# Performance work log

Hardware: AMD Instinct MI355X
Metric: run time of the kernel (lower is better)

The kernel has to match this reference:

```python
import jax, jax.numpy as jnp
import numpy as np

D = 1024      # d_model
B = 8         # batch
S = 512       # seq
L = 2         # GRU layers
DEPTH = 3     # min_depth == max_depth -> fixed recursion depth
EPS_RMS = 1.1920929e-07  # torch fp32 finfo eps (nn.RMSNorm default)


def setup_inputs() -> dict:
    key = jax.random.key(0)
    ks = jax.random.split(key, 16)

    def glorot(k, shape):
        fan_out, fan_in = shape
        lim = float(np.sqrt(6.0 / (fan_in + fan_out)))
        return jax.random.uniform(k, shape, jnp.float32, -lim, lim)

    gs = float(1.0 / np.sqrt(D))  # torch GRU init: U(-1/sqrt(H), 1/sqrt(H))
    inp = {
        "x": jax.random.normal(ks[0], (B, S, D), jnp.float32),
        # reflect: Linear -> RMSNorm -> GELU -> Linear -> RMSNorm
        "w1": glorot(ks[1], (D, D)), "b1": jnp.zeros(D, jnp.float32),
        "rms1_w": jnp.ones(D, jnp.float32),
        "w2": glorot(ks[2], (D, D)), "b2": jnp.zeros(D, jnp.float32),
        "rms2_w": jnp.ones(D, jnp.float32),
        "residual_weight": jnp.float32(0.5),
        # IntegrationMeasure projections (xavier_uniform, zero bias)
        "whole_w": glorot(ks[3], (D // 2, D)), "whole_b": jnp.zeros(D // 2, jnp.float32),
        "parts_w": glorot(ks[4], (D // 2, D)), "parts_b": jnp.zeros(D // 2, jnp.float32),
        "phi_scale": jnp.float32(1.0), "phi_bias": jnp.float32(0.0),
    }
    ki = 5
    for l in range(L):
        inp[f"wih{l}"] = jax.random.uniform(ks[ki + 0], (3 * D, D), jnp.float32, -gs, gs)
        inp[f"whh{l}"] = jax.random.uniform(ks[ki + 1], (3 * D, D), jnp.float32, -gs, gs)
        inp[f"bih{l}"] = jax.random.uniform(ks[ki + 2], (3 * D,), jnp.float32, -gs, gs)
        inp[f"bhh{l}"] = jax.random.uniform(ks[ki + 3], (3 * D,), jnp.float32, -gs, gs)
        ki += 4
    return inp


def _rmsnorm(x, w):
    ms = jnp.mean(x * x, axis=-1, keepdims=True)
    return x * jax.lax.rsqrt(ms + EPS_RMS) * w


def _gru_layer(seq, h0, Wih, Whh, bih, bhh):
    """seq: [S,B,D], h0: [B,D] -> (outputs [S,B,D], h_final [B,D]). torch gate order r,z,n."""
    def step(h, xt):
        gi = xt @ Wih.T + bih                       # [B, 3D]
        gh = h @ Whh.T + bhh                        # [B, 3D]
        ir, iz, ig = jnp.split(gi, 3, axis=-1)
        hr, hz, hg = jnp.split(gh, 3, axis=-1)
        r = jax.nn.sigmoid(ir + hr)
        z = jax.nn.sigmoid(iz + hz)
        n = jnp.tanh(ig + r * hg)
        hn = (1.0 - z) * n + z * h
        return hn, hn
    hT, ys = jax.lax.scan(step, h0, seq)
    return ys, hT


def reference(x, w1, b1, rms1_w, w2, b2, rms2_w, residual_weight,
              wih0, whh0, bih0, bhh0, wih1, whh1, bih1, bhh1,
              whole_w, whole_b, parts_w, parts_b, phi_scale, phi_bias):
    gru = [(wih0, whh0, bih0, bhh0), (wih1, whh1, bih1, bhh1)]
    batch = x.shape[0]
    hidden = [jnp.zeros((batch, D), x.dtype) for _ in range(L)]
    history = []  # detached states
    phi = None

    for loop in range(DEPTH):
        # self-reflection block
        h = _rmsnorm(x @ w1.T + b1, rms1_w)
        h = jax.nn.gelu(h, approximate=False)
        h = _rmsnorm(h @ w2.T + b2, rms2_w)
        x_ref = x + residual_weight * (h - x)
        # GRU integration (seq-first)
        seq = jnp.transpose(x_ref, (1, 0, 2))       # [S,B,D]
        new_hidden = []
        for l in range(L):
            seq, hT = _gru_layer(seq, hidden[l], *gru[l])
            new_hidden.append(hT)
        hidden = new_hidden
        x = jnp.transpose(seq, (0, 1, 2)).transpose(1, 0, 2)  # [B,S,D]
        # Phi (IntegrationMeasure) -- manifold_norm == L2 norm, fully vectorized
        whole = x @ whole_w.T + whole_b             # [B,S,D/2]
        whole_info = jnp.linalg.norm(whole, axis=-1).mean(axis=-1)  # [B]
        if len(history) == 0:
            phi = jnp.broadcast_to(jax.nn.sigmoid(phi_bias) * 0.3, (batch,))
        else:
            parts = jnp.stack(history) @ parts_w.T + parts_b      # [H,B,S,D/2]
            parts_info = jnp.linalg.norm(parts, axis=-1).mean(axis=-1).mean(axis=0)  # [B]
            raw_phi = (whole_info - parts_info) / (whole_info + 1e-08)
            phi = jnp.clip(phi_scale * raw_phi + phi_bias, 0.0, 1.0)
        history.append(jax.lax.stop_gradient(x))    # torch: x.clone().detach()

    return x, phi
```

## Files before the change

### kernel.cpp

```cpp
#include <hip/hip_runtime.h>
#include <math.h>

#define Dm 1024
#define Bm 8
#define Sm 512

typedef short s16x8 __attribute__((ext_vector_type(8)));
typedef float f32x4 __attribute__((ext_vector_type(4)));
typedef unsigned short u16;
typedef unsigned long long u64;

__device__ __forceinline__ float bf2f(u16 u) {
  union { float f; unsigned v; } x; x.v = (unsigned)u << 16; return x.f;
}
__device__ __forceinline__ u16 f2bf(float f) {
  union { float f; unsigned v; } x; x.f = f;
  unsigned r = x.v + 0x7FFFu + ((x.v >> 16) & 1u);
  return (u16)(r >> 16);
}
__device__ __forceinline__ float sigm(float x) { return 1.f / (1.f + expf(-x)); }

__device__ __forceinline__ u64 cld64(const void* p) {
  return __hip_atomic_load((const u64*)p, __ATOMIC_RELAXED, __HIP_MEMORY_SCOPE_AGENT);
}
__device__ __forceinline__ float cldf(const void* p) {
  return __hip_atomic_load((const float*)p, __ATOMIC_RELAXED, __HIP_MEMORY_SCOPE_AGENT);
}
__device__ __forceinline__ void cx64(void* p, u64 v) {
  u64 old = __hip_atomic_exchange((u64*)p, v, __ATOMIC_RELAXED, __HIP_MEMORY_SCOPE_AGENT);
  asm volatile("" :: "v"(old));
}
__device__ __forceinline__ void cst32(void* p, unsigned v) {
  __hip_atomic_store((unsigned*)p, v, __ATOMIC_RELAXED, __HIP_MEMORY_SCOPE_AGENT);
}

__global__ void k_conv(const float* __restrict__ x, const float* __restrict__ w1,
                       const float* __restrict__ w2, const float* __restrict__ ww,
                       const float* __restrict__ pw,
                       u16* __restrict__ Xb, u16* __restrict__ Wc,
                       float* __restrict__ Hf, u16* __restrict__ Hb,
                       float* __restrict__ sums, unsigned* __restrict__ flags,
                       unsigned* __restrict__ poison)
{
  long gid = (long)blockIdx.x * blockDim.x + threadIdx.x;
  const long N0 = 4194304, N1 = 1048576, N2 = 1048576, N3 = 524288, N4 = 524288;
  const long T = N0 + N1 + N2 + N3 + N4;
  for (long p = gid; p < T; p += (long)gridDim.x * blockDim.x) {
    long q = p;
    if (q < N0) { Xb[q] = f2bf(x[q]); continue; }
    q -= N0;
    if (q < N1) { Wc[q] = f2bf(w1[q]); continue; }
    q -= N1;
    if (q < N2) { Wc[N1 + q] = f2bf(w2[q]); continue; }
    q -= N2;
    if (q < N3) { Wc[N1 + N2 + q] = f2bf(ww[q]); continue; }
    q -= N3;
    Wc[N1 + N2 + N3 + q] = f2bf(pw[q]);
  }
  if (gid < 65536) flags[gid] = 0;
  if (gid < 2 * Bm * Dm) Hf[gid] = 0.f;
  if (gid < 262144) Hb[gid] = 0;
  if (gid < 16) sums[gid] = 0.f;
  if (gid == 0) *poison = 0;
}

template<int MODE>
__global__ __launch_bounds__(512)
void k_gemm(const u16* __restrict__ A, const u16* __restrict__ W,
            const float* __restrict__ bias, const float* __restrict__ nw,
            const u16* __restrict__ XresB, const float* __restrict__ rwp,
            u16* __restrict__ out0, float* __restrict__ sumdst, int Ncols)
{
  __shared__ u16 At[16 * 1024];
  __shared__ float rowsq[16];
  const int tid = threadIdx.x;
  const int lane = tid & 63, wv = tid >> 6;
  const int rlo = lane & 15, khi = lane >> 4;
  const int m0 = blockIdx.x * 16;

  {
    int row = tid & 15, c = tid >> 4;
    const char* src = (const char*)(A + (long)(m0 + row) * Dm);
    char* dst = (char*)At + row * 2048;
    int sw = (row & 7) << 4;
#pragma unroll
    for (int i = 0; i < 4; ++i) {
      int bo = c * 64 + i * 16;
      s16x8 v = *(const s16x8*)(src + bo);
      *(s16x8*)(dst + (bo ^ sw)) = v;
    }
  }
  __syncthreads();

  const int j0 = wv * 128;
  const bool act = j0 < Ncols;
  f32x4 zero4 = {0.f, 0.f, 0.f, 0.f};
  f32x4 acc[8];
#pragma unroll
  for (int jt = 0; jt < 8; ++jt) acc[jt] = zero4;

  if (act) {
    const u16* wbase = W + (long)(j0 + rlo) * Dm + khi * 8;
    const char* abase = (const char*)At + rlo * 2048;
    const int asw = (rlo & 7) << 4;
#pragma unroll
    for (int ks = 0; ks < 32; ++ks) {
      s16x8 a = *(const s16x8*)(abase + (((ks * 32 + khi * 8) * 2) ^ asw));
#pragma unroll
      for (int jt = 0; jt < 8; ++jt) {
        s16x8 b = *(const s16x8*)(wbase + (long)jt * 16 * Dm + ks * 32);
        acc[jt] = __builtin_amdgcn_mfma_f32_16x16x32_bf16(a, b, acc[jt], 0, 0, 0);
      }
    }
  }

  if (tid < 16) rowsq[tid] = 0.f;
  __syncthreads();

  float vals[8][4];
  if (act) {
    float rs[4] = {0.f, 0.f, 0.f, 0.f};
#pragma unroll
    for (int jt = 0; jt < 8; ++jt) {
      float bj = bias[j0 + jt * 16 + rlo];
#pragma unroll
      for (int r = 0; r < 4; ++r) {
        float v = acc[jt][r] + bj;
        vals[jt][r] = v;
        rs[r] += v * v;
      }
    }
#pragma unroll
    for (int r = 0; r < 4; ++r) {
#pragma unroll
      for (int m = 1; m < 16; m <<= 1) rs[r] += __shfl_xor(rs[r], m, 64);
    }
    if (rlo == 0) {
#pragma unroll
      for (int r = 0; r < 4; ++r) atomicAdd(&rowsq[khi * 4 + r], rs[r]);
    }
  }
  __syncthreads();

  if constexpr (MODE == 2) {
    if (tid < 16) {
      int token = m0 + tid;
      atomicAdd(&sumdst[token >> 9], sqrtf(rowsq[tid]));
    }
    return;
  } else {
    float rw = 0.f;
    if constexpr (MODE == 1) rw = rwp[0];
    if (act) {
#pragma unroll
      for (int jt = 0; jt < 8; ++jt) {
        int col = j0 + jt * 16 + rlo;
        float nwv = nw[col];
#pragma unroll
        for (int r = 0; r < 4; ++r) {
          int row = khi * 4 + r;
          int token = m0 + row;
          float ms = rowsq[row] * (1.f / 1024.f) + 1.1920929e-07f;
          float y = vals[jt][r] * rsqrtf(ms) * nwv;
          if constexpr (MODE == 0) {
            y = 0.5f * y * (1.f + erff(y * 0.7071067811865476f));
            out0[(long)token * Dm + col] = f2bf(y);
          } else {
            float xf = bf2f(XresB[(long)token * Dm + col]);
            float xr = xf + rw * (y - xf);
            u16 hi = f2bf(xr);
            float lo = xr - bf2f(hi);
            int s = token & (Sm - 1), b = token >> 9;
            long base = ((long)s * 16 + b) * Dm + col;
            out0[base] = hi;
            out0[base + 8 * Dm] = f2bf(lo);
          }
        }
      }
    }
  }
}

#define SPIN_CAP 2000000

__device__ __forceinline__ bool spin_all(const unsigned* pA, const unsigned* pB,
                                         unsigned val, unsigned* poison) {
  int spins = 0;
  while (true) {
    bool c = __hip_atomic_load(pA, __ATOMIC_RELAXED, __HIP_MEMORY_SCOPE_AGENT) >= val;
    if (pB) c = c && (__hip_atomic_load(pB, __ATOMIC_RELAXED, __HIP_MEMORY_SCOPE_AGENT) >= val);
    if (__all(c)) return true;
    __builtin_amdgcn_s_sleep(1);
    if ((++spins & 255) == 0) {
      if (__hip_atomic_load(poison, __ATOMIC_RELAXED, __HIP_MEMORY_SCOPE_AGENT)) return false;
      if (spins > SPIN_CAP) {
        __hip_atomic_store(poison, 1u, __ATOMIC_RELAXED, __HIP_MEMORY_SCOPE_AGENT);
        return false;
      }
    }
  }
}

__global__ __launch_bounds__(256, 1)
void k_rec(const float* __restrict__ wih0, const float* __restrict__ whh0,
           const float* __restrict__ bih0, const float* __restrict__ bhh0,
           const float* __restrict__ wih1, const float* __restrict__ whh1,
           const float* __restrict__ bih1, const float* __restrict__ bhh1,
           const u16* __restrict__ XrefB,
           float* __restrict__ gi0r, float* __restrict__ gi1r,
           u16* __restrict__ Hb, float* __restrict__ Hf,
           u16* __restrict__ Xb, float* __restrict__ outx,
           unsigned* __restrict__ flags, unsigned* __restrict__ poison, int loop)
{
  __shared__ u16 hbuf[16 * 1024];
  __shared__ float part[4][3][16][33];

  const int wg = blockIdx.x;
  const int role = wg >> 5;
  const int w = wg & 31;
  const int d0 = w * 32;
  const int tid = threadIdx.x;
  const int lane = tid & 63, q = tid >> 6;
  const int rlo = lane & 15, khi = lane >> 4;
  const unsigned val = (unsigned)loop + 1u;

  unsigned* F0 = flags;
  unsigned* F1 = flags + 16384;
  unsigned* F2 = flags + 32768;
  unsigned* F3 = flags + 49152;
  u16* Hb0 = Hb;
  u16* Hb1 = Hb + 8 * 16384;

  const float* Wsel = (role == 0) ? wih0 : (role == 1) ? whh0 : (role == 2) ? wih1 : whh1;

  s16x8 bfr[8][3][2];
#pragma unroll
  for (int ks = 0; ks < 8; ++ks)
#pragma unroll
    for (int g = 0; g < 3; ++g)
#pragma unroll
      for (int jt = 0; jt < 2; ++jt) {
        int rowj = g * 1024 + d0 + jt * 16 + rlo;
        const float* p = Wsel + (long)rowj * Dm + q * 256 + ks * 32 + khi * 8;
        s16x8 f;
#pragma unroll
        for (int e = 0; e < 8; ++e) f[e] = (short)f2bf(p[e]);
        bfr[ks][g][jt] = f;
      }

  const int ob = tid >> 5, odd = tid & 31, od = d0 + odd;
  float bias_r[3];
  {
    const float* bsel = (role == 0) ? bih0 : (role == 1) ? bhh0 : (role == 2) ? bih1 : bhh1;
#pragma unroll
    for (int g = 0; g < 3; ++g) bias_r[g] = bsel[g * 1024 + od];
  }
  const int layer = (role == 1) ? 0 : 1;
  float hreg = 0.f;
  if (role == 1 || role == 3) hreg = Hf[layer * 8192 + ob * 1024 + od];
  __syncthreads();

  for (int t = 0; t < Sm; ++t) {
    if (role == 0) {
      if (t >= 8) { if (!spin_all(&F1[(t - 8) * 32 + w], nullptr, val, poison)) return; }
    } else if (role == 1) {
      const unsigned* fb = &F0[t * 32 + w];
      const unsigned* pA =
          (lane < 32) ? ((t >= 1) ? &F1[(t - 1) * 32 + lane] : fb)
                      : ((t >= 8) ? &F2[(t - 8) * 32 + (lane - 32)] : fb);
      if (!spin_all(pA, fb, val, poison)) return;
    } else if (role == 2) {
      const unsigned* pA =
          (lane < 32) ? &F1[t * 32 + lane]
                      : ((t >= 8) ? &F3[(t - 8) * 32 + (lane - 32)] : &F1[t * 32 + (lane - 32)]);
      if (!spin_all(pA, nullptr, val, poison)) return;
    } else {
      const unsigned* fb = &F2[t * 32 + w];
      const unsigned* pA = (lane < 32) ? ((t >= 1) ? &F3[(t - 1) * 32 + lane] : fb) : fb;
      if (!spin_all(pA, fb, val, poison)) return;
    }
    __builtin_amdgcn_sched_barrier(0);

    float giv[3] = {0.f, 0.f, 0.f};
    if (role == 1 || role == 3) {
      const float* ring = ((role == 1) ? gi0r : gi1r) + ((long)(t & 7) * Bm + ob) * 3072 + od;
      giv[0] = cldf(ring);
      giv[1] = cldf(ring + 1024);
      giv[2] = cldf(ring + 2048);
    }
    __syncthreads();

    if (role == 0) {
      const u16* asrc = XrefB + (long)t * 16 * Dm;
      int row = tid & 15, c = tid >> 4;
      const char* src = (const char*)(asrc + row * Dm);
      char* dst = (char*)hbuf + row * 2048;
      int sw = (row & 7) << 4;
#pragma unroll
      for (int i = 0; i < 8; ++i) {
        int bo = c * 128 + i * 16;
        s16x8 v = *(const s16x8*)(src + bo);
        *(s16x8*)(dst + (bo ^ sw)) = v;
      }
    } else {
      const u16* asrc =
          (role == 1) ? Hb0 + ((t - 1) & 7) * 16384 :
          (role == 2) ? Hb0 + (t & 7) * 16384 :
                        Hb1 + ((t - 1) & 7) * 16384;
      int row = tid & 15, c = tid >> 4;
      const u16* src = asrc + row * 1024 + c * 64;
      char* dst = (char*)hbuf + row * 2048;
      int sw = (row & 7) << 4;
#pragma unroll
      for (int i = 0; i < 16; ++i) {
        u64 v = cld64(src + i * 4);
        int bo = c * 128 + i * 8;
        *(u64*)(dst + (bo ^ sw)) = v;
      }
    }
    __syncthreads();

    f32x4 zero4 = {0.f, 0.f, 0.f, 0.f};
    f32x4 acc[3][2];
#pragma unroll
    for (int g = 0; g < 3; ++g) { acc[g][0] = zero4; acc[g][1] = zero4; }
    const char* abase = (const char*)hbuf + rlo * 2048;
    const int asw = (rlo & 7) << 4;
#pragma unroll
    for (int ks = 0; ks < 8; ++ks) {
      s16x8 a = *(const s16x8*)(abase + (((q * 256 + ks * 32 + khi * 8) * 2) ^ asw));
#pragma unroll
      for (int g = 0; g < 3; ++g)
#pragma unroll
        for (int jt = 0; jt < 2; ++jt)
          acc[g][jt] = __builtin_amdgcn_mfma_f32_16x16x32_bf16(a, bfr[ks][g][jt], acc[g][jt], 0, 0, 0);
    }
#pragma unroll
    for (int g = 0; g < 3; ++g)
#pragma unroll
      for (int jt = 0; jt < 2; ++jt)
#pragma unroll
        for (int r = 0; r < 4; ++r)
          part[q][g][khi * 4 + r][jt * 16 + rlo] = acc[g][jt][r];
    __syncthreads();

    {
      int b = ob, dd = odd, d = od;
      float v[3];
#pragma unroll
      for (int g = 0; g < 3; ++g) {
        float sv = 0.f;
#pragma unroll
        for (int qq = 0; qq < 4; ++qq)
          sv += part[qq][g][b][dd] + part[qq][g][8 + b][dd];
        v[g] = sv;
      }
      if (role == 0 || role == 2) {
        float* ring = ((role == 0) ? gi0r : gi1r) + ((long)(t & 7) * Bm + b) * 3072 + d;
#pragma unroll
        for (int g = 0; g < 3; ++g) {
          float fg = v[g] + bias_r[g];
          float pg = __shfl_xor(fg, 1, 64);
          if ((dd & 1) == 0) {
            union { float f; unsigned u; } a0, a1;
            a0.f = fg; a1.f = pg;
            u64 pk = (u64)a0.u | ((u64)a1.u << 32);
            cx64(ring + g * 1024, pk);
          }
        }
      } else {
        float gr = giv[0] + v[0] + bias_r[0];
        float gz = giv[1] + v[1] + bias_r[1];
        float ghn = v[2] + bias_r[2];
        float rr = sigm(gr), zz = sigm(gz);
        float nn = tanhf(giv[2] + rr * ghn);
        float hn = (1.f - zz) * nn + zz * hreg;
        hreg = hn;
        u16 hi = f2bf(hn);
        u16 lo = f2bf(hn - bf2f(hi));
        unsigned myv = (unsigned)hi | ((unsigned)lo << 16);
        unsigned p1 = __shfl_xor(myv, 1, 64);
        unsigned hiPair = (myv & 0xFFFFu) | ((p1 & 0xFFFFu) << 16);
        unsigned loPair = (myv >> 16) | (p1 & 0xFFFF0000u);
        unsigned hp2 = __shfl_xor(hiPair, 2, 64);
        unsigned lp2 = __shfl_xor(loPair, 2, 64);
        if ((dd & 3) == 0) {
          u64 hq = (u64)hiPair | ((u64)hp2 << 32);
          u64 lq = (u64)loPair | ((u64)lp2 << 32);
          u16* hb = ((role == 1) ? Hb0 : Hb1) + (t & 7) * 16384;
          cx64(hb + b * 1024 + d, hq);
          cx64(hb + 8192 + b * 1024 + d, lq);
        }
        if (role == 3) {
          long xi = ((long)b * Sm + t) * Dm + d;
          Xb[xi] = hi;
          if (outx) outx[xi] = hn;
        }
        if (t == Sm - 1) Hf[layer * 8192 + b * 1024 + d] = hreg;
      }
    }
    __syncthreads();
    __builtin_amdgcn_sched_barrier(0);
    if (tid == 0) {
      unsigned* F = (role == 0) ? F0 : (role == 1) ? F1 : (role == 2) ? F2 : F3;
      cst32(&F[t * 32 + w], val);
    }
  }
}

__global__ void k_phi(const float* __restrict__ sums, const float* __restrict__ psc,
                      const float* __restrict__ pbi, float* __restrict__ out)
{
  int b = threadIdx.x;
  if (b < 8) {
    float whole = sums[8 + b] * (1.f / 512.f);
    float parts = sums[b] * (1.f / 1024.f);
    float raw = (whole - parts) / (whole + 1e-8f);
    float phi = psc[0] * raw + pbi[0];
    phi = fminf(fmaxf(phi, 0.f), 1.f);
    out[(long)Bm * Sm * Dm + b] = phi;
  }
}

extern "C" void kernel_launch(void* const* d_in, const int* in_sizes, int n_in,
                              void* d_out, int out_size, void* d_ws, size_t ws_size,
                              hipStream_t stream)
{
  (void)in_sizes; (void)n_in; (void)out_size;
  const float* b1   = (const float*)d_in[2];
  const float* r1w  = (const float*)d_in[3];
  const float* b2   = (const float*)d_in[5];
  const float* r2w  = (const float*)d_in[6];
  const float* rw   = (const float*)d_in[7];
  const float* wb   = (const float*)d_in[9];
  const float* pb   = (const float*)d_in[11];
  const float* psc  = (const float*)d_in[12];
  const float* pbi  = (const float*)d_in[13];
  const float* wih0 = (const float*)d_in[14];
  const float* whh0 = (const float*)d_in[15];
  const float* bih0 = (const float*)d_in[16];
  const float* bhh0 = (const float*)d_in[17];
  const float* wih1 = (const float*)d_in[18];
  const float* whh1 = (const float*)d_in[19];
  const float* bih1 = (const float*)d_in[20];
  const float* bhh1 = (const float*)d_in[21];
  float* out = (float*)d_out;

  if (ws_size < 45000000) return;

  char* ws = (char*)d_ws;
  size_t off = 0;
  auto alloc = [&](size_t bytes) -> char* {
    char* p = ws + off;
    off += (bytes + 255) & ~(size_t)255;
    return p;
  };
  u16*      Xb    = (u16*)  alloc((size_t)4194304 * 2);
  u16*      T1    = (u16*)  alloc((size_t)4194304 * 2);
  u16*      XrefB = (u16*)  alloc((size_t)2 * 4194304 * 2);
  float*    gi0r  = (float*)alloc((size_t)8 * 8 * 3072 * 4);
  float*    gi1r  = (float*)alloc((size_t)8 * 8 * 3072 * 4);
  u16*      Hb    = (u16*)  alloc((size_t)2 * 8 * 16384 * 2);
  float*    Hf    = (float*)alloc((size_t)2 * 8192 * 4);
  u16*      Wc    = (u16*)  alloc((size_t)3145728 * 2);
  float*    sums  = (float*)alloc(16 * 4);
  unsigned* flags = (unsigned*)alloc((size_t)65536 * 4);
  unsigned* poi   = (unsigned*)alloc(256);

  u16* WcW1 = Wc;
  u16* WcW2 = Wc + 1048576;
  u16* WcWW = Wc + 2097152;
  u16* WcPW = Wc + 2621440;

  k_conv<<<2048, 256, 0, stream>>>((const float*)d_in[0], (const float*)d_in[1],
                                   (const float*)d_in[4], (const float*)d_in[8],
                                   (const float*)d_in[10],
                                   Xb, Wc, Hf, Hb, sums, flags, poi);

  for (int loop = 0; loop < 3; ++loop) {
    k_gemm<0><<<256, 512, 0, stream>>>(Xb, WcW1, b1, r1w, nullptr, nullptr, T1, nullptr, 1024);
    k_gemm<1><<<256, 512, 0, stream>>>(T1, WcW2, b2, r2w, Xb, rw, XrefB, nullptr, 1024);
    k_rec<<<128, 256, 0, stream>>>(wih0, whh0, bih0, bhh0, wih1, whh1, bih1, bhh1,
                                   XrefB, gi0r, gi1r, Hb, Hf, Xb,
                                   (loop == 2) ? out : nullptr, flags, poi, loop);
    if (loop < 2)
      k_gemm<2><<<256, 512, 0, stream>>>(Xb, WcPW, pb, nullptr, nullptr, nullptr, nullptr, sums, 512);
    else
      k_gemm<2><<<256, 512, 0, stream>>>(Xb, WcWW, wb, nullptr, nullptr, nullptr, nullptr, sums + 8, 512);
  }
  k_phi<<<1, 64, 0, stream>>>(sums, psc, pbi, out);
}
```

Measured before the change: 12.40 ms.

## Merge input and hidden GRU projections into one workgroup per layer slice

The persistent recurrent kernel drops from four roles (input-proj and hidden-proj per layer) to two, with each workgroup holding both Wih and Whh fragments in registers and computing both projections for its slice. This removes the gi ring buffers in global memory and one level of cross-workgroup flag handoff per timestep, which shortens the serial dependency chain. In exchange it doubles register pressure for the weight fragments and the MFMA work per workgroup, and halves the number of active workgroups. Only one wave now spins on flags, and a shared-memory poison flag propagates an abort to the rest of the block.

```diff
diff --git a/kernel.cpp b/kernel.cpp
--- a/kernel.cpp
+++ b/kernel.cpp
@@ -22,9 +22,6 @@
 
 __device__ __forceinline__ u64 cld64(const void* p) {
   return __hip_atomic_load((const u64*)p, __ATOMIC_RELAXED, __HIP_MEMORY_SCOPE_AGENT);
-}
-__device__ __forceinline__ float cldf(const void* p) {
-  return __hip_atomic_load((const float*)p, __ATOMIC_RELAXED, __HIP_MEMORY_SCOPE_AGENT);
 }
 __device__ __forceinline__ void cx64(void* p, u64 v) {
   u64 old = __hip_atomic_exchange((u64*)p, v, __ATOMIC_RELAXED, __HIP_MEMORY_SCOPE_AGENT);
@@ -57,7 +54,7 @@
     q -= N3;
     Wc[N1 + N2 + N3 + q] = f2bf(pw[q]);
   }
-  if (gid < 65536) flags[gid] = 0;
+  if (gid < 32768) flags[gid] = 0;
   if (gid < 2 * Bm * Dm) Hf[gid] = 0.f;
   if (gid < 262144) Hb[gid] = 0;
   if (gid < 16) sums[gid] = 0.f;
@@ -183,12 +180,11 @@
 
 #define SPIN_CAP 2000000
 
-__device__ __forceinline__ bool spin_all(const unsigned* pA, const unsigned* pB,
-                                         unsigned val, unsigned* poison) {
+__device__ __forceinline__ bool spin_en(const unsigned* p, bool en, unsigned val,
+                                        unsigned* poison) {
   int spins = 0;
   while (true) {
-    bool c = __hip_atomic_load(pA, __ATOMIC_RELAXED, __HIP_MEMORY_SCOPE_AGENT) >= val;
-    if (pB) c = c && (__hip_atomic_load(pB, __ATOMIC_RELAXED, __HIP_MEMORY_SCOPE_AGENT) >= val);
+    bool c = !en || (__hip_atomic_load(p, __ATOMIC_RELAXED, __HIP_MEMORY_SCOPE_AGENT) >= val);
     if (__all(c)) return true;
     __builtin_amdgcn_s_sleep(1);
     if ((++spins & 255) == 0) {
@@ -207,13 +203,14 @@
            const float* __restrict__ wih1, const float* __restrict__ whh1,
            const float* __restrict__ bih1, const float* __restrict__ bhh1,
            const u16* __restrict__ XrefB,
-           float* __restrict__ gi0r, float* __restrict__ gi1r,
            u16* __restrict__ Hb, float* __restrict__ Hf,
            u16* __restrict__ Xb, float* __restrict__ outx,
            unsigned* __restrict__ flags, unsigned* __restrict__ poison, int loop)
 {
-  __shared__ u16 hbuf[16 * 1024];
-  __shared__ float part[4][3][16][33];
+  __shared__ u16 hbufI[16 * 1024];
+  __shared__ u16 hbufH[16 * 1024];
+  __shared__ float part[4][4][16][33];
+  __shared__ unsigned pflag;
 
   const int wg = blockIdx.x;
   const int role = wg >> 5;
@@ -224,16 +221,17 @@
   const int rlo = lane & 15, khi = lane >> 4;
   const unsigned val = (unsigned)loop + 1u;
 
-  unsigned* F0 = flags;
-  unsigned* F1 = flags + 16384;
-  unsigned* F2 = flags + 32768;
-  unsigned* F3 = flags + 49152;
+  unsigned* F1 = flags;
+  unsigned* F3 = flags + 16384;
   u16* Hb0 = Hb;
   u16* Hb1 = Hb + 8 * 16384;
 
-  const float* Wsel = (role == 0) ? wih0 : (role == 1) ? whh0 : (role == 2) ? wih1 : whh1;
-
-  s16x8 bfr[8][3][2];
+  if (tid == 0) pflag = 0;
+
+  const float* WI = role ? wih1 : wih0;
+  const float* WH = role ? whh1 : whh0;
+
+  s16x8 fI[8][3][2], fH[8][3][2];
 #pragma unroll
   for (int ks = 0; ks < 8; ++ks)
 #pragma unroll
@@ -241,60 +239,51 @@
 #pragma unroll
       for (int jt = 0; jt < 2; ++jt) {
         int rowj = g * 1024 + d0 + jt * 16 + rlo;
-        const float* p = Wsel + (long)rowj * Dm + q * 256 + ks * 32 + khi * 8;
-        s16x8 f;
-#pragma unroll
-        for (int e = 0; e < 8; ++e) f[e] = (short)f2bf(p[e]);
-        bfr[ks][g][jt] = f;
+        long boff = (long)rowj * Dm + q * 256 + ks * 32 + khi * 8;
+        const float* pI = WI + boff;
+        const float* pH = WH + boff;
+        s16x8 a, b;
+#pragma unroll
+        for (int e = 0; e < 8; ++e) { a[e] = (short)f2bf(pI[e]); b[e] = (short)f2bf(pH[e]); }
+        fI[ks][g][jt] = a;
+        fH[ks][g][jt] = b;
       }
 
   const int ob = tid >> 5, odd = tid & 31, od = d0 + odd;
-  float bias_r[3];
-  {
-    const float* bsel = (role == 0) ? bih0 : (role == 1) ? bhh0 : (role == 2) ? bih1 : bhh1;
-#pragma unroll
-    for (int g = 0; g < 3; ++g) bias_r[g] = bsel[g * 1024 + od];
-  }
-  const int layer = (role == 1) ? 0 : 1;
-  float hreg = 0.f;
-  if (role == 1 || role == 3) hreg = Hf[layer * 8192 + ob * 1024 + od];
+  const float* bI = role ? bih1 : bih0;
+  const float* bH = role ? bhh1 : bhh0;
+  float bias_r = bI[od] + bH[od];
+  float bias_z = bI[1024 + od] + bH[1024 + od];
+  float bias_ni = bI[2048 + od];
+  float bias_nh = bH[2048 + od];
+  float hreg = Hf[role * 8192 + ob * 1024 + od];
   __syncthreads();
 
   for (int t = 0; t < Sm; ++t) {
-    if (role == 0) {
-      if (t >= 8) { if (!spin_all(&F1[(t - 8) * 32 + w], nullptr, val, poison)) return; }
-    } else if (role == 1) {
-      const unsigned* fb = &F0[t * 32 + w];
-      const unsigned* pA =
-          (lane < 32) ? ((t >= 1) ? &F1[(t - 1) * 32 + lane] : fb)
-                      : ((t >= 8) ? &F2[(t - 8) * 32 + (lane - 32)] : fb);
-      if (!spin_all(pA, fb, val, poison)) return;
-    } else if (role == 2) {
-      const unsigned* pA =
-          (lane < 32) ? &F1[t * 32 + lane]
-                      : ((t >= 8) ? &F3[(t - 8) * 32 + (lane - 32)] : &F1[t * 32 + (lane - 32)]);
-      if (!spin_all(pA, nullptr, val, poison)) return;
-    } else {
-      const unsigned* fb = &F2[t * 32 + w];
-      const unsigned* pA = (lane < 32) ? ((t >= 1) ? &F3[(t - 1) * 32 + lane] : fb) : fb;
-      if (!spin_all(pA, fb, val, poison)) return;
+    if (q == 0) {
+      const unsigned* p;
+      bool en;
+      if (role == 0) {
+        int tm1 = (t >= 1) ? t - 1 : 0;
+        int tm8 = (t >= 8) ? t - 8 : 0;
+        p = (lane < 32) ? &F1[tm1 * 32 + lane] : &F3[tm8 * 32 + (lane - 32)];
+        en = (lane < 32) ? (t >= 1) : (t >= 8);
+      } else {
+        int sm1 = (t >= 1) ? t - 1 : 0;
+        p = (lane < 32) ? &F1[t * 32 + lane] : &F3[sm1 * 32 + (lane - 32)];
+        en = (lane < 32) ? true : (t >= 1);
+      }
+      if (!spin_en(p, en, val, poison)) { if (lane == 0) pflag = 1; }
     }
     __builtin_amdgcn_sched_barrier(0);
-
-    float giv[3] = {0.f, 0.f, 0.f};
-    if (role == 1 || role == 3) {
-      const float* ring = ((role == 1) ? gi0r : gi1r) + ((long)(t & 7) * Bm + ob) * 3072 + od;
-      giv[0] = cldf(ring);
-      giv[1] = cldf(ring + 1024);
-      giv[2] = cldf(ring + 2048);
-    }
     __syncthreads();
+    if (pflag) return;
 
     if (role == 0) {
       const u16* asrc = XrefB + (long)t * 16 * Dm;
       int row = tid & 15, c = tid >> 4;
       const char* src = (const char*)(asrc + row * Dm);
-      char* dst = (char*)hbuf + row * 2048;
+      char* dst = (char*)hbufI + row * 2048;
       int sw = (row & 7) << 4;
 #pragma unroll
       for (int i = 0; i < 8; ++i) {
@@ -303,13 +292,10 @@
         *(s16x8*)(dst + (bo ^ sw)) = v;
       }
     } else {
-      const u16* asrc =
-          (role == 1) ? Hb0 + ((t - 1) & 7) * 16384 :
-          (role == 2) ? Hb0 + (t & 7) * 16384 :
-                        Hb1 + ((t - 1) & 7) * 16384;
+      const u16* asrc = Hb0 + (t & 7) * 16384;
       int row = tid & 15, c = tid >> 4;
       const u16* src = asrc + row * 1024 + c * 64;
-      char* dst = (char*)hbuf + row * 2048;
+      char* dst = (char*)hbufI + row * 2048;
       int sw = (row & 7) << 4;
 #pragma unroll
       for (int i = 0; i < 16; ++i) {
@@ -318,91 +304,96 @@
         *(u64*)(dst + (bo ^ sw)) = v;
       }
     }
+    {
+      const u16* asrc = (role ? Hb1 : Hb0) + ((t - 1) & 7) * 16384;
+      int row = tid & 15, c = tid >> 4;
+      const u16* src = asrc + row * 1024 + c * 64;
+      char* dst = (char*)hbufH + row * 2048;
+      int sw = (row & 7) << 4;
+#pragma unroll
+      for (int i = 0; i < 16; ++i) {
+        u64 v = cld64(src + i * 4);
+        int bo = c * 128 + i * 8;
+        *(u64*)(dst + (bo ^ sw)) = v;
+      }
+    }
     __syncthreads();
 
     f32x4 zero4 = {0.f, 0.f, 0.f, 0.f};
-    f32x4 acc[3][2];
-#pragma unroll
-    for (int g = 0; g < 3; ++g) { acc[g][0] = zero4; acc[g][1] = zero4; }
-    const char* abase = (const char*)hbuf + rlo * 2048;
+    f32x4 accR[2], accZ[2], accNI[2], accNH[2];
+#pragma unroll
+    for (int jt = 0; jt < 2; ++jt) { accR[jt] = zero4; accZ[jt] = zero4; accNI[jt] = zero4; accNH[jt] = zero4; }
+    const char* aIb = (const char*)hbufI + rlo * 2048;
+    const char* aHb = (const char*)hbufH + rlo * 2048;
     const int asw = (rlo & 7) << 4;
 #pragma unroll
     for (int ks = 0; ks < 8; ++ks) {
-      s16x8 a = *(const s16x8*)(abase + (((q * 256 + ks * 32 + khi * 8) * 2) ^ asw));
-#pragma unroll
-      for (int g = 0; g < 3; ++g)
-#pragma unroll
-        for (int jt = 0; jt < 2; ++jt)
-          acc[g][jt] = __builtin_amdgcn_mfma_f32_16x16x32_bf16(a, bfr[ks][g][jt], acc[g][jt], 0, 0, 0);
-    }
-#pragma unroll
-    for (int g = 0; g < 3; ++g)
-#pragma unroll
-      for (int jt = 0; jt < 2; ++jt)
-#pragma unroll
-        for (int r = 0; r < 4; ++r)
-          part[q][g][khi * 4 + r][jt * 16 + rlo] = acc[g][jt][r];
+      int ao = (((q * 256 + ks * 32 + khi * 8) * 2)) ;
+      s16x8 aI = *(const s16x8*)(aIb + (ao ^ asw));
+      s16x8 aH = *(const s16x8*)(aHb + (ao ^ asw));
+#pragma unroll
+      for (int jt = 0; jt < 2; ++jt) {
+        accR[jt] = __builtin_amdgcn_mfma_f32_16x16x32_bf16(aI, fI[ks][0][jt], accR[jt], 0, 0, 0);
+        accR[jt] = __builtin_amdgcn_mfma_f32_16x16x32_bf16(aH, fH[ks][0][jt], accR[jt], 0, 0, 0);
+        accZ[jt] = __builtin_amdgcn_mfma_f32_16x16x32_bf16(aI, fI[ks][1][jt], accZ[jt], 0, 0, 0);
+        accZ[jt] = __builtin_amdgcn_mfma_f32_16x16x32_bf16(aH, fH[ks][1][jt], accZ[jt], 0, 0, 0);
+        accNI[jt] = __builtin_amdgcn_mfma_f32_16x16x32_bf16(aI, fI[ks][2][jt], accNI[jt], 0, 0, 0);
+        accNH[jt] = __builtin_amdgcn_mfma_f32_16x16x32_bf16(aH, fH[ks][2][jt], accNH[jt], 0, 0, 0);
+      }
+    }
+#pragma unroll
+    for (int jt = 0; jt < 2; ++jt)
+#pragma unroll
+      for (int r = 0; r < 4; ++r) {
+        part[q][0][khi * 4 + r][jt * 16 + rlo] = accR[jt][r];
+        part[q][1][khi * 4 + r][jt * 16 + rlo] = accZ[jt][r];
+        part[q][2][khi * 4 + r][jt * 16 + rlo] = accNI[jt][r];
+        part[q][3][khi * 4 + r][jt * 16 + rlo] = accNH[jt][r];
+      }
     __syncthreads();
 
     {
-      int b = ob, dd = odd, d = od;
-      float v[3];
-#pragma unroll
-      for (int g = 0; g < 3; ++g) {
+      int b = ob, dd = odd;
+      float v[4];
+#pragma unroll
+      for (int g = 0; g < 4; ++g) {
         float sv = 0.f;
 #pragma unroll
         for (int qq = 0; qq < 4; ++qq)
           sv += part[qq][g][b][dd] + part[qq][g][8 + b][dd];
         v[g] = sv;
       }
-      if (role == 0 || role == 2) {
-        float* ring = ((role == 0) ? gi0r : gi1r) + ((long)(t & 7) * Bm + b) * 3072 + d;
-#pragma unroll
-        for (int g = 0; g < 3; ++g) {
-          float fg = v[g] + bias_r[g];
-          float pg = __shfl_xor(fg, 1, 64);
-          if ((dd & 1) == 0) {
-            union { float f; unsigned u; } a0, a1;
-            a0.f = fg; a1.f = pg;
-            u64 pk = (u64)a0.u | ((u64)a1.u << 32);
-            cx64(ring + g * 1024, pk);
-          }
-        }
-      } else {
-        float gr = giv[0] + v[0] + bias_r[0];
-        float gz = giv[1] + v[1] + bias_r[1];
-        float ghn = v[2] + bias_r[2];
-        float rr = sigm(gr), zz = sigm(gz);
-        float nn = tanhf(giv[2] + rr * ghn);
-        float hn = (1.f - zz) * nn + zz * hreg;
-        hreg = hn;
-        u16 hi = f2bf(hn);
-        u16 lo = f2bf(hn - bf2f(hi));
-        unsigned myv = (unsigned)hi | ((unsigned)lo << 16);
-        unsigned p1 = __shfl_xor(myv, 1, 64);
-        unsigned hiPair = (myv & 0xFFFFu) | ((p1 & 0xFFFFu) << 16);
-        unsigned loPair = (myv >> 16) | (p1 & 0xFFFF0000u);
-        unsigned hp2 = __shfl_xor(hiPair, 2, 64);
-        unsigned lp2 = __shfl_xor(loPair, 2, 64);
-        if ((dd & 3) == 0) {
-          u64 hq = (u64)hiPair | ((u64)hp2 << 32);
-          u64 lq = (u64)loPair | ((u64)lp2 << 32);
-          u16* hb = ((role == 1) ? Hb0 : Hb1) + (t & 7) * 16384;
-          cx64(hb + b * 1024 + d, hq);
-          cx64(hb + 8192 + b * 1024 + d, lq);
-        }
-        if (role == 3) {
-          long xi = ((long)b * Sm + t) * Dm + d;
-          Xb[xi] = hi;
-          if (outx) outx[xi] = hn;
-        }
-        if (t == Sm - 1) Hf[layer * 8192 + b * 1024 + d] = hreg;
-      }
+      float rr = sigm(v[0] + bias_r);
+      float zz = sigm(v[1] + bias_z);
+      float nn = tanhf(v[2] + bias_ni + rr * (v[3] + bias_nh));
+      float hn = (1.f - zz) * nn + zz * hreg;
+      hreg = hn;
+      u16 hi = f2bf(hn);
+      u16 lo = f2bf(hn - bf2f(hi));
+      unsigned myv = (unsigned)hi | ((unsigned)lo << 16);
+      unsigned p1 = __shfl_xor(myv, 1, 64);
+      unsigned hiPair = (myv & 0xFFFFu) | ((p1 & 0xFFFFu) << 16);
+      unsigned loPair = (myv >> 16) | (p1 & 0xFFFF0000u);
+      unsigned hp2 = __shfl_xor(hiPair, 2, 64);
+      unsigned lp2 = __shfl_xor(loPair, 2, 64);
+      if ((dd & 3) == 0) {
+        u64 hq = (u64)hiPair | ((u64)hp2 << 32);
+        u64 lq = (u64)loPair | ((u64)lp2 << 32);
+        u16* hb = (role ? Hb1 : Hb0) + (t & 7) * 16384;
+        cx64(hb + b * 1024 + od, hq);
+        cx64(hb + 8192 + b * 1024 + od, lq);
+      }
+      if (role == 1) {
+        long xi = ((long)b * Sm + t) * Dm + od;
+        Xb[xi] = hi;
+        if (outx) outx[xi] = hn;
+      }
+      if (t == Sm - 1) Hf[role * 8192 + b * 1024 + od] = hreg;
     }
     __syncthreads();
     __builtin_amdgcn_sched_barrier(0);
     if (tid == 0) {
-      unsigned* F = (role == 0) ? F0 : (role == 1) ? F1 : (role == 2) ? F2 : F3;
+      unsigned* F = role ? F3 : F1;
       cst32(&F[t * 32 + w], val);
     }
   }
@@ -458,13 +449,11 @@
   u16*      Xb    = (u16*)  alloc((size_t)4194304 * 2);
   u16*      T1    = (u16*)  alloc((size_t)4194304 * 2);
   u16*      XrefB = (u16*)  alloc((size_t)2 * 4194304 * 2);
-  float*    gi0r  = (float*)alloc((size_t)8 * 8 * 3072 * 4);
-  float*    gi1r  = (float*)alloc((size_t)8 * 8 * 3072 * 4);
   u16*      Hb    = (u16*)  alloc((size_t)2 * 8 * 16384 * 2);
   float*    Hf    = (float*)alloc((size_t)2 * 8192 * 4);
   u16*      Wc    = (u16*)  alloc((size_t)3145728 * 2);
   float*    sums  = (float*)alloc(16 * 4);
-  unsigned* flags = (unsigned*)alloc((size_t)65536 * 4);
+  unsigned* flags = (unsigned*)alloc((size_t)32768 * 4);
   unsigned* poi   = (unsigned*)alloc(256);
 
   u16* WcW1 = Wc;
@@ -480,9 +469,9 @@
   for (int loop = 0; loop < 3; ++loop) {
     k_gemm<0><<<256, 512, 0, stream>>>(Xb, WcW1, b1, r1w, nullptr, nullptr, T1, nullptr, 1024);
     k_gemm<1><<<256, 512, 0, stream>>>(T1, WcW2, b2, r2w, Xb, rw, XrefB, nullptr, 1024);
-    k_rec<<<128, 256, 0, stream>>>(wih0, whh0, bih0, bhh0, wih1, whh1, bih1, bhh1,
-                                   XrefB, gi0r, gi1r, Hb, Hf, Xb,
-                                   (loop == 2) ? out : nullptr, flags, poi, loop);
+    k_rec<<<64, 256, 0, stream>>>(wih0, whh0, bih0, bhh0, wih1, whh1, bih1, bhh1,
+                                  XrefB, Hb, Hf, Xb,
+                                  (loop == 2) ? out : nullptr, flags, poi, loop);
     if (loop < 2)
       k_gemm<2><<<256, 512, 0, stream>>>(Xb, WcPW, pb, nullptr, nullptr, nullptr, nullptr, sums, 512);
     else
```

Result: slower. 15.13 ms (+22.0%).

## Load GRU A-operand directly into registers and spin on flags with one wave

Applied to the files above, without the earlier changes.

Each wave now loads its MFMA A fragments straight from global memory into registers instead of staging the 16x1024 activation tile through swizzled LDS. This removes the LDS round trip and one barrier per timestep. Only wave 0 polls the inter-block flags; it reports poison through a shared flag and a single barrier releases the other waves. The cost is more uncoalesced global loads per lane, since each of the four waves reads its own K slice, and a possible bank or latency effect on the critical recurrent path.

```diff
diff --git a/kernel.cpp b/kernel.cpp
--- a/kernel.cpp
+++ b/kernel.cpp
@@ -183,11 +183,11 @@
 
 #define SPIN_CAP 2000000
 
-__device__ __forceinline__ bool spin_all(const unsigned* pA, const unsigned* pB,
-                                         unsigned val, unsigned* poison) {
+__device__ __forceinline__ bool spin2(const unsigned* pA, bool enA, const unsigned* pB,
+                                      unsigned val, unsigned* poison) {
   int spins = 0;
   while (true) {
-    bool c = __hip_atomic_load(pA, __ATOMIC_RELAXED, __HIP_MEMORY_SCOPE_AGENT) >= val;
+    bool c = !enA || (__hip_atomic_load(pA, __ATOMIC_RELAXED, __HIP_MEMORY_SCOPE_AGENT) >= val);
     if (pB) c = c && (__hip_atomic_load(pB, __ATOMIC_RELAXED, __HIP_MEMORY_SCOPE_AGENT) >= val);
     if (__all(c)) return true;
     __builtin_amdgcn_s_sleep(1);
@@ -212,8 +212,8 @@
            u16* __restrict__ Xb, float* __restrict__ outx,
            unsigned* __restrict__ flags, unsigned* __restrict__ poison, int loop)
 {
-  __shared__ u16 hbuf[16 * 1024];
   __shared__ float part[4][3][16][33];
+  __shared__ unsigned pflag;
 
   const int wg = blockIdx.x;
   const int role = wg >> 5;
@@ -231,6 +231,8 @@
   u16* Hb0 = Hb;
   u16* Hb1 = Hb + 8 * 16384;
 
+  if (tid == 0) pflag = 0;
+
   const float* Wsel = (role == 0) ? wih0 : (role == 1) ? whh0 : (role == 2) ? wih1 : whh1;
 
   s16x8 bfr[8][3][2];
@@ -261,25 +263,36 @@
   __syncthreads();
 
   for (int t = 0; t < Sm; ++t) {
-    if (role == 0) {
-      if (t >= 8) { if (!spin_all(&F1[(t - 8) * 32 + w], nullptr, val, poison)) return; }
-    } else if (role == 1) {
-      const unsigned* fb = &F0[t * 32 + w];
-      const unsigned* pA =
-          (lane < 32) ? ((t >= 1) ? &F1[(t - 1) * 32 + lane] : fb)
-                      : ((t >= 8) ? &F2[(t - 8) * 32 + (lane - 32)] : fb);
-      if (!spin_all(pA, fb, val, poison)) return;
-    } else if (role == 2) {
-      const unsigned* pA =
-          (lane < 32) ? &F1[t * 32 + lane]
-                      : ((t >= 8) ? &F3[(t - 8) * 32 + (lane - 32)] : &F1[t * 32 + (lane - 32)]);
-      if (!spin_all(pA, nullptr, val, poison)) return;
-    } else {
-      const unsigned* fb = &F2[t * 32 + w];
-      const unsigned* pA = (lane < 32) ? ((t >= 1) ? &F3[(t - 1) * 32 + lane] : fb) : fb;
-      if (!spin_all(pA, fb, val, poison)) return;
+    if (q == 0) {
+      const unsigned* pA;
+      const unsigned* pB = nullptr;
+      bool enA;
+      bool need = true;
+      if (role == 0) {
+        pA = &F1[((t >= 8) ? (t - 8) : 0) * 32 + w];
+        enA = true;
+        need = (t >= 8);
+      } else if (role == 1) {
+        pA = (lane < 32) ? &F1[((t >= 1) ? (t - 1) : 0) * 32 + lane]
+                         : &F2[((t >= 8) ? (t - 8) : 0) * 32 + (lane - 32)];
+        enA = (lane < 32) ? (t >= 1) : (t >= 8);
+        pB = &F0[t * 32 + w];
+      } else if (role == 2) {
+        pA = (lane < 32) ? &F1[t * 32 + lane]
+                         : &F3[((t >= 8) ? (t - 8) : 0) * 32 + (lane - 32)];
+        enA = (lane < 32) ? true : (t >= 8);
+      } else {
+        pA = &F3[((t >= 1) ? (t - 1) : 0) * 32 + ((lane < 32) ? lane : (lane - 32))];
+        enA = (lane < 32) && (t >= 1);
+        pB = &F2[t * 32 + w];
+      }
+      if (need) {
+        if (!spin2(pA, enA, pB, val, poison)) { if (lane == 0) pflag = 1; }
+      }
     }
     __builtin_amdgcn_sched_barrier(0);
+    __syncthreads();
+    if (pflag) return;
 
     float giv[3] = {0.f, 0.f, 0.f};
     if (role == 1 || role == 3) {
@@ -288,53 +301,39 @@
       giv[1] = cldf(ring + 1024);
       giv[2] = cldf(ring + 2048);
     }
-    __syncthreads();
-
+
+    s16x8 areg[8];
     if (role == 0) {
-      const u16* asrc = XrefB + (long)t * 16 * Dm;
-      int row = tid & 15, c = tid >> 4;
-      const char* src = (const char*)(asrc + row * Dm);
-      char* dst = (char*)hbuf + row * 2048;
-      int sw = (row & 7) << 4;
-#pragma unroll
-      for (int i = 0; i < 8; ++i) {
-        int bo = c * 128 + i * 16;
-        s16x8 v = *(const s16x8*)(src + bo);
-        *(s16x8*)(dst + (bo ^ sw)) = v;
-      }
+      const u16* src = XrefB + (long)t * 16 * Dm + rlo * 1024 + q * 256 + khi * 8;
+#pragma unroll
+      for (int ks = 0; ks < 8; ++ks)
+        areg[ks] = *(const s16x8*)(src + ks * 32);
     } else {
-      const u16* asrc =
-          (role == 1) ? Hb0 + ((t - 1) & 7) * 16384 :
-          (role == 2) ? Hb0 + (t & 7) * 16384 :
-                        Hb1 + ((t - 1) & 7) * 16384;
-      int row = tid & 15, c = tid >> 4;
-      const u16* src = asrc + row * 1024 + c * 64;
-      char* dst = (char*)hbuf + row * 2048;
-      int sw = (row & 7) << 4;
-#pragma unroll
-      for (int i = 0; i < 16; ++i) {
-        u64 v = cld64(src + i * 4);
-        int bo = c * 128 + i * 8;
-        *(u64*)(dst + (bo ^ sw)) = v;
-      }
-    }
-    __syncthreads();
+      const u16* base = (role == 1) ? Hb0 + ((t - 1) & 7) * 16384
+                      : (role == 2) ? Hb0 + (t & 7) * 16384
+                                    : Hb1 + ((t - 1) & 7) * 16384;
+      const u16* src = base + rlo * 1024 + q * 256 + khi * 8;
+#pragma unroll
+      for (int ks = 0; ks < 8; ++ks) {
+        union { u64 u[2]; s16x8 v; } tmp;
+        tmp.u[0] = cld64(src + ks * 32);
+        tmp.u[1] = cld64(src + ks * 32 + 4);
+        areg[ks] = tmp.v;
+      }
+    }
 
     f32x4 zero4 = {0.f, 0.f, 0.f, 0.f};
     f32x4 acc[3][2];
 #pragma unroll
     for (int g = 0; g < 3; ++g) { acc[g][0] = zero4; acc[g][1] = zero4; }
-    const char* abase = (const char*)hbuf + rlo * 2048;
-    const int asw = (rlo & 7) << 4;
-#pragma unroll
-    for (int ks = 0; ks < 8; ++ks) {
-      s16x8 a = *(const s16x8*)(abase + (((q * 256 + ks * 32 + khi * 8) * 2) ^ asw));
+#pragma unroll
+    for (int ks = 0; ks < 8; ++ks)
 #pragma unroll
       for (int g = 0; g < 3; ++g)
 #pragma unroll
         for (int jt = 0; jt < 2; ++jt)
-          acc[g][jt] = __builtin_amdgcn_mfma_f32_16x16x32_bf16(a, bfr[ks][g][jt], acc[g][jt], 0, 0, 0);
-    }
+          acc[g][jt] = __builtin_amdgcn_mfma_f32_16x16x32_bf16(areg[ks], bfr[ks][g][jt], acc[g][jt], 0, 0, 0);
+
 #pragma unroll
     for (int g = 0; g < 3; ++g)
 #pragma unroll
@@ -345,7 +344,7 @@
     __syncthreads();
 
     {
-      int b = ob, dd = odd, d = od;
+      int b = ob, dd = odd;
       float v[3];
 #pragma unroll
       for (int g = 0; g < 3; ++g) {
@@ -356,7 +355,7 @@
         v[g] = sv;
       }
       if (role == 0 || role == 2) {
-        float* ring = ((role == 0) ? gi0r : gi1r) + ((long)(t & 7) * Bm + b) * 3072 + d;
+        float* ring = ((role == 0) ? gi0r : gi1r) + ((long)(t & 7) * Bm + b) * 3072 + od;
 #pragma unroll
         for (int g = 0; g < 3; ++g) {
           float fg = v[g] + bias_r[g];
@@ -388,15 +387,15 @@
           u64 hq = (u64)hiPair | ((u64)hp2 << 32);
           u64 lq = (u64)loPair | ((u64)lp2 << 32);
           u16* hb = ((role == 1) ? Hb0 : Hb1) + (t & 7) * 16384;
-          cx64(hb + b * 1024 + d, hq);
-          cx64(hb + 8192 + b * 1024 + d, lq);
+          cx64(hb + b * 1024 + od, hq);
+          cx64(hb + 8192 + b * 1024 + od, lq);
         }
         if (role == 3) {
-          long xi = ((long)b * Sm + t) * Dm + d;
+          long xi = ((long)b * Sm + t) * Dm + od;
           Xb[xi] = hi;
           if (outx) outx[xi] = hn;
         }
-        if (t == Sm - 1) Hf[layer * 8192 + b * 1024 + d] = hreg;
+        if (t == Sm - 1) Hf[layer * 8192 + b * 1024 + od] = hreg;
       }
     }
     __syncthreads();
```

After: 10.67 ms. 1.16x faster.
